# Optimization experiments

Hardware: AMD Instinct MI355X
Metric: run time of the kernel (lower is better)

The kernel has to match this reference:

```python
import jax, jax.numpy as jnp
import numpy as np

N_PROP = 1000
N_CLS = 81  # includes background class 0
IMG_H, IMG_W = 800, 1333
WX, WY, WW, WH = 10.0, 10.0, 5.0, 5.0
BBOX_XFORM_CLIP = float(np.log(1000.0 / 16.0))
SCORE_THRESH = 0.05
NMS_THRESH = 0.5
DET_PER_IMG = 100


def _decode(box_regression, proposals):
    widths = proposals[:, 2] - proposals[:, 0] + 1.0
    heights = proposals[:, 3] - proposals[:, 1] + 1.0
    ctr_x = proposals[:, 0] + 0.5 * widths
    ctr_y = proposals[:, 1] + 0.5 * heights
    rel = box_regression.reshape(box_regression.shape[0], -1, 4)  # [N, C, 4]
    dx = rel[..., 0] / WX
    dy = rel[..., 1] / WY
    dw = jnp.minimum(rel[..., 2] / WW, BBOX_XFORM_CLIP)
    dh = jnp.minimum(rel[..., 3] / WH, BBOX_XFORM_CLIP)
    pcx = dx * widths[:, None] + ctr_x[:, None]
    pcy = dy * heights[:, None] + ctr_y[:, None]
    pw = jnp.exp(dw) * widths[:, None]
    ph = jnp.exp(dh) * heights[:, None]
    return jnp.stack([pcx - 0.5 * pw, pcy - 0.5 * ph,
                      pcx + 0.5 * pw - 1.0, pcy + 0.5 * ph - 1.0], axis=-1)  # [N, C, 4]


def _clip_boxes(b, h, w):
    x1 = jnp.clip(b[..., 0], 0.0, w - 1.0)
    y1 = jnp.clip(b[..., 1], 0.0, h - 1.0)
    x2 = jnp.clip(b[..., 2], 0.0, w - 1.0)
    y2 = jnp.clip(b[..., 3], 0.0, h - 1.0)
    return jnp.stack([x1, y1, x2, y2], axis=-1)


def _nms_keep(boxes, scores, valid):
    # Greedy NMS for one class. boxes [N,4], scores [N], valid [N].
    # Returns keep mask in the ORIGINAL proposal order.
    n = scores.shape[0]
    order = jnp.argsort(-jnp.where(valid, scores, -jnp.inf))
    b = boxes[order]
    v = valid[order]
    x1, y1, x2, y2 = b[:, 0], b[:, 1], b[:, 2], b[:, 3]
    area = (x2 - x1 + 1.0) * (y2 - y1 + 1.0)
    iw = jnp.clip(jnp.minimum(x2[:, None], x2[None, :]) - jnp.maximum(x1[:, None], x1[None, :]) + 1.0, 0.0)
    ih = jnp.clip(jnp.minimum(y2[:, None], y2[None, :]) - jnp.maximum(y1[:, None], y1[None, :]) + 1.0, 0.0)
    inter = iw * ih
    iou = inter / (area[:, None] + area[None, :] - inter)
    idx = jnp.arange(n)

    def body(i, keep):
        sup = (iou[i] > NMS_THRESH) & (idx > i) & keep[i]
        return keep & ~sup

    keep = jax.lax.fori_loop(0, n, body, v)
    return jnp.zeros(n, dtype=bool).at[order].set(keep)


def _postprocess(class_logits, box_regression, proposal_boxes, image_h, image_w):
    prob = jax.nn.softmax(class_logits, axis=-1)             # [N, C]
    boxes = _decode(box_regression, proposal_boxes)           # [N, C, 4]
    boxes = _clip_boxes(boxes, float(image_h), float(image_w))
    scores_c = prob[:, 1:].T                                  # [C-1, N] skip background
    boxes_c = jnp.transpose(boxes[:, 1:, :], (1, 0, 2))       # [C-1, N, 4]
    valid = scores_c > SCORE_THRESH
    keep = jax.vmap(_nms_keep)(boxes_c, scores_c, valid)      # [C-1, N]
    masked = jnp.where(keep, scores_c, -jnp.inf)
    count = jnp.sum(keep)
    # torch.kthvalue(n - 100) == 101st largest kept score; keep scores >= it
    topv = jax.lax.top_k(masked.reshape(-1), DET_PER_IMG + 1)[0]
    image_thresh = jnp.where(count > DET_PER_IMG, topv[DET_PER_IMG], -jnp.inf)
    final = keep & (masked >= image_thresh)
    c1, n = scores_c.shape
    labels = jnp.broadcast_to(jnp.arange(1, c1 + 1, dtype=jnp.int32)[:, None], (c1, n))
    out_scores = jnp.where(final, scores_c, 0.0).reshape(-1)
    out_boxes = jnp.where(final[..., None], boxes_c, 0.0).reshape(-1, 4)
    out5 = jnp.concatenate([out_boxes, out_scores[:, None]], axis=1)  # [(C-1)*N, 5]
    return out5, jnp.where(final, labels, 0).reshape(-1), final.reshape(-1)


def setup_inputs() -> dict:
    key = jax.random.key(0)
    k1, k2, k3, k4 = jax.random.split(key, 4)
    # scale logits so a realistic fraction of softmax scores clears the 0.05 threshold
    class_logits = 3.0 * jax.random.normal(k1, (N_PROP, N_CLS), dtype=jnp.float32)
    box_regression = jax.random.normal(k2, (N_PROP, N_CLS * 4), dtype=jnp.float32)
    cxy = jax.random.uniform(k3, (N_PROP, 2), dtype=jnp.float32) * jnp.array([IMG_W, IMG_H], jnp.float32)
    wh = 16.0 + 284.0 * jax.random.uniform(k4, (N_PROP, 2), dtype=jnp.float32)
    x1y1 = jnp.clip(cxy - 0.5 * wh, 0.0)
    x2y2 = jnp.minimum(cxy + 0.5 * wh, jnp.array([IMG_W - 1.0, IMG_H - 1.0], jnp.float32))
    proposal_boxes = jnp.concatenate([x1y1, x2y2], axis=1)  # [N, 4] xyxy
    return {"class_logits": class_logits, "box_regression": box_regression,
            "proposal_boxes": proposal_boxes, "image_h": IMG_H, "image_w": IMG_W}


def reference(class_logits, box_regression, proposal_boxes, image_h, image_w):
    return _postprocess(class_logits, box_regression, proposal_boxes, image_h, image_w)
```

## Files before the change

kernel.cpp:

```cpp
#include <hip/hip_runtime.h>
#include <math.h>

#define N_PROP 1000
#define N_CLS  81
#define N_FG   80
#define SCORE_THRESH 0.05f
#define NMS_THRESH   0.5f
#define DET_PER_IMG  100
#define BBOX_CLIP    4.135166556742356f

#define LBL_OFF    400000
#define FIN_OFF    480000


__global__ __launch_bounds__(256)
void softmax_zero_kernel(const float* __restrict__ logits,
                         float* __restrict__ out,
                         int* __restrict__ count,
                         float* __restrict__ probT) {
    const int b = blockIdx.x;
    const int t = threadIdx.x;
    const int lane = t & 63;
    const int wave = t >> 6;
    if (b == 0 && t == 0) *count = 0;

    float4 z = make_float4(0.f, 0.f, 0.f, 0.f);
    float4* o4 = (float4*)out;
    for (int i = b * 256 + t; i < 140000; i += 250 * 256) o4[i] = z;

    const int n = b * 4 + wave;
    if (n < N_PROP) {
        const float* lrow = logits + (size_t)n * N_CLS;
        float v0 = lrow[lane];
        float v1 = (lane + 64 < N_CLS) ? lrow[lane + 64] : -INFINITY;
        float m = fmaxf(v0, v1);
        for (int off = 32; off; off >>= 1) m = fmaxf(m, __shfl_down(m, off));
        m = __shfl(m, 0);
        float e0 = expf(v0 - m);
        float e1 = (lane + 64 < N_CLS) ? expf(v1 - m) : 0.0f;
        float s = e0 + e1;
        for (int off = 32; off; off >>= 1) s += __shfl_down(s, off);
        s = __shfl(s, 0);
        if (lane >= 1)          probT[(size_t)(lane - 1) * N_PROP + n] = e0 / s;
        if (lane + 64 < N_CLS)  probT[(size_t)(lane + 63) * N_PROP + n] = e1 / s;
    }
}

__global__ __launch_bounds__(256)
void nms_kernel(const float* __restrict__ probT,
                const float* __restrict__ props,
                const float* __restrict__ reg,
                const int* __restrict__ ihp,
                const int* __restrict__ iwp,
                float* __restrict__ out,
                int* __restrict__ count,
                float* __restrict__ compact,
                int* __restrict__ svRow) {
    const int c = blockIdx.x;
    const int t = threadIdx.x;
    const int lane = t & 63;
    const int cls = c + 1;
    const unsigned long long lm = (1ull << lane) - 1ull;

    __shared__ float sSc[N_PROP];
    __shared__ int   sIdx[N_PROP];
    __shared__ int   sPos[N_PROP];
    __shared__ float sx1[N_PROP], sy1[N_PROP], sx2[N_PROP], sy2[N_PROP];
    __shared__ float sar[N_PROP], sSc2[N_PROP];
    __shared__ int   sJdx[N_PROP];
    __shared__ unsigned char sKeep[N_PROP];
    __shared__ unsigned long long sColMask[128][2];
    __shared__ int   shV;

    for (int j = t; j < N_PROP; j += 256) sSc[j] = probT[(size_t)c * N_PROP + j];
    __syncthreads();

    if (t < 64) {
        int V = 0;
        #pragma unroll
        for (int it = 0; it < 16; ++it) {
            int j = it * 64 + lane;
            float sc = (j < N_PROP) ? sSc[j] : -1.0f;
            bool val = (j < N_PROP) && (sc > SCORE_THRESH);
            unsigned long long mask = __ballot(val);
            if (val) { int p = V + __popcll(mask & lm); sSc[p] = sc; sIdx[p] = j; }
            V += __popcll(mask);
        }
        if (lane == 0) shV = V;
    }
    __syncthreads();
    const int V = shV;

    const float W1 = (float)iwp[0] - 1.0f;
    const float H1 = (float)ihp[0] - 1.0f;

    if (V <= 128) {
        if (t < V) {
            float s = sSc[t];
            int id = sIdx[t];
            int r = 0;
            for (int u = 0; u < V; ++u) {
                float su = sSc[u];
                r += (su > s) || (su == s && sIdx[u] < id);
            }
            float4 pr = *(const float4*)(props + (size_t)id * 4);
            float w  = pr.z - pr.x + 1.0f;
            float h  = pr.w - pr.y + 1.0f;
            float cx = pr.x + 0.5f * w;
            float cy = pr.y + 0.5f * h;
            float4 rr = *(const float4*)(reg + ((size_t)id * N_CLS + cls) * 4);
            float dx = rr.x / 10.0f;
            float dy = rr.y / 10.0f;
            float dw = fminf(rr.z / 5.0f, BBOX_CLIP);
            float dh = fminf(rr.w / 5.0f, BBOX_CLIP);
            float pcx = dx * w + cx;
            float pcy = dy * h + cy;
            float pw = expf(dw) * w;
            float ph = expf(dh) * h;
            float bx1 = fminf(fmaxf(pcx - 0.5f * pw, 0.0f), W1);
            float by1 = fminf(fmaxf(pcy - 0.5f * ph, 0.0f), H1);
            float bx2 = fminf(fmaxf(pcx + 0.5f * pw - 1.0f, 0.0f), W1);
            float by2 = fminf(fmaxf(pcy + 0.5f * ph - 1.0f, 0.0f), H1);
            sx1[r] = bx1; sy1[r] = by1; sx2[r] = bx2; sy2[r] = by2;
            sar[r] = (bx2 - bx1 + 1.0f) * (by2 - by1 + 1.0f);
            sSc2[r] = s;
            sJdx[r] = id;
        }
        __syncthreads();

        if (t < V) {
            const float X1 = sx1[t], Y1 = sy1[t], X2 = sx2[t], Y2 = sy2[t], A = sar[t];
            unsigned long long m0 = 0ull, m1 = 0ull;
            for (int r = 0; r < t; ++r) {
                float iw = fmaxf(fminf(sx2[r], X2) - fmaxf(sx1[r], X1) + 1.0f, 0.0f);
                float ih = fmaxf(fminf(sy2[r], Y2) - fmaxf(sy1[r], Y1) + 1.0f, 0.0f);
                float inter = iw * ih;
                float iou = inter / (sar[r] + A - inter);
                if (iou > NMS_THRESH) {
                    if (r < 64) m0 |= 1ull << r; else m1 |= 1ull << (r - 64);
                }
            }
            sColMask[t][0] = m0;
            sColMask[t][1] = m1;
        }
        __syncthreads();

        if (t < 64) {
            const bool hasA = (lane < V), hasB = (64 + lane < V);
            unsigned long long Mlo = 0ull, M2lo = 0ull, M2hi = 0ull;
            if (hasA) Mlo  = sColMask[lane][0];
            if (hasB) { M2lo = sColMask[64 + lane][0]; M2hi = sColMask[64 + lane][1]; }

            unsigned long long keep = 0ull, keep2 = 0ull;
            bool a = hasA, a2 = hasB;
            while (true) {
                unsigned long long b1 = __ballot(a);
                unsigned long long b2 = __ballot(a2);
                if (!(b1 | b2)) break;
                int r = b1 ? (__ffsll((long long)b1) - 1) : (64 + __ffsll((long long)b2) - 1);
                if (r < 64) {
                    keep |= 1ull << r;
                    if (a  && ((Mlo  >> r) & 1ull)) a  = false;
                    if (a2 && ((M2lo >> r) & 1ull)) a2 = false;
                    if (lane == r) a = false;
                } else {
                    int rr = r - 64;
                    keep2 |= 1ull << rr;
                    if (a2 && ((M2hi >> rr) & 1ull)) a2 = false;
                    if (lane == rr) a2 = false;
                }
            }

            int total = __popcll(keep) + __popcll(keep2);
            int base = 0;
            if (lane == 0 && total > 0) base = atomicAdd(count, total);
            base = __shfl(base, 0);
            if ((keep >> lane) & 1ull) {
                float sc = sSc2[lane];
                int row = c * N_PROP + sJdx[lane];
                size_t o = (size_t)row * 5;
                out[o + 0] = sx1[lane]; out[o + 1] = sy1[lane];
                out[o + 2] = sx2[lane]; out[o + 3] = sy2[lane];
                out[o + 4] = sc;
                out[LBL_OFF + row] = (float)cls;
                out[FIN_OFF + row] = 1.0f;
                int pos = base + __popcll(keep & lm);
                compact[pos] = sc; svRow[pos] = row;
            }
            if ((keep2 >> lane) & 1ull) {
                float sc = sSc2[64 + lane];
                int row = c * N_PROP + sJdx[64 + lane];
                size_t o = (size_t)row * 5;
                out[o + 0] = sx1[64 + lane]; out[o + 1] = sy1[64 + lane];
                out[o + 2] = sx2[64 + lane]; out[o + 3] = sy2[64 + lane];
                out[o + 4] = sc;
                out[LBL_OFF + row] = (float)cls;
                out[FIN_OFF + row] = 1.0f;
                int pos = base + __popcll(keep) + __popcll(keep2 & lm);
                compact[pos] = sc; svRow[pos] = row;
            }
        }
    } else {
        for (int v = t; v < V; v += 256) {
            float s = sSc[v];
            int id = sIdx[v];
            int r = 0;
            for (int u = 0; u < V; ++u) {
                float su = sSc[u];
                r += (su > s) || (su == s && sIdx[u] < id);
            }
            sPos[v] = r;
        }
        __syncthreads();
        for (int v = t; v < V; v += 256) {
            int r = sPos[v];
            int j = sIdx[v];
            float4 pr = *(const float4*)(props + (size_t)j * 4);
            float w  = pr.z - pr.x + 1.0f;
            float h  = pr.w - pr.y + 1.0f;
            float cx = pr.x + 0.5f * w;
            float cy = pr.y + 0.5f * h;
            float4 rr = *(const float4*)(reg + ((size_t)j * N_CLS + cls) * 4);
            float dx = rr.x / 10.0f;
            float dy = rr.y / 10.0f;
            float dw = fminf(rr.z / 5.0f, BBOX_CLIP);
            float dh = fminf(rr.w / 5.0f, BBOX_CLIP);
            float pcx = dx * w + cx;
            float pcy = dy * h + cy;
            float pw = expf(dw) * w;
            float ph = expf(dh) * h;
            float bx1 = fminf(fmaxf(pcx - 0.5f * pw, 0.0f), W1);
            float by1 = fminf(fmaxf(pcy - 0.5f * ph, 0.0f), H1);
            float bx2 = fminf(fmaxf(pcx + 0.5f * pw - 1.0f, 0.0f), W1);
            float by2 = fminf(fmaxf(pcy + 0.5f * ph - 1.0f, 0.0f), H1);
            sx1[r] = bx1; sy1[r] = by1; sx2[r] = bx2; sy2[r] = by2;
            sar[r] = (bx2 - bx1 + 1.0f) * (by2 - by1 + 1.0f);
            sSc2[r] = sSc[v];
            sJdx[r] = j;
            sKeep[r] = 1;
        }
        __syncthreads();
        for (int r = 0; r < V; ++r) {
            if (sKeep[r]) {
                const float X1 = sx1[r], Y1 = sy1[r], X2 = sx2[r], Y2 = sy2[r], A = sar[r];
                for (int v = r + 1 + t; v < V; v += 256) {
                    if (sKeep[v]) {
                        float iw = fmaxf(fminf(X2, sx2[v]) - fmaxf(X1, sx1[v]) + 1.0f, 0.0f);
                        float ih = fmaxf(fminf(Y2, sy2[v]) - fmaxf(Y1, sy1[v]) + 1.0f, 0.0f);
                        float inter = iw * ih;
                        float iou = inter / (A + sar[v] - inter);
                        if (iou > NMS_THRESH) sKeep[v] = 0;
                    }
                }
            }
            __syncthreads();
        }
        for (int vb = 0; vb < V; vb += 256) {
            int v = vb + t;
            bool k = (v < V) && sKeep[v];
            unsigned long long mask = __ballot(k);
            int cntw = __popcll(mask);
            int base = 0;
            if (lane == 0 && cntw > 0) base = atomicAdd(count, cntw);
            base = __shfl(base, 0);
            if (k) {
                int row = c * N_PROP + sJdx[v];
                size_t o = (size_t)row * 5;
                out[o + 0] = sx1[v]; out[o + 1] = sy1[v];
                out[o + 2] = sx2[v]; out[o + 3] = sy2[v];
                out[o + 4] = sSc2[v];
                out[LBL_OFF + row] = (float)cls;
                out[FIN_OFF + row] = 1.0f;
                int pos = base + __popcll(mask & lm);
                compact[pos] = sSc2[v];
                svRow[pos] = row;
            }
        }
    }
}

__global__ __launch_bounds__(256)
void finalize_kernel(float* __restrict__ out,
                     const float* __restrict__ compact,
                     const int* __restrict__ svRow,
                     const int* __restrict__ count) {
    __shared__ float lsc[8192];
    __shared__ float sTh;
    const int n = *count;
    const int t = threadIdx.x;
    const int lane = t & 63;

    if (n <= DET_PER_IMG) return;

    const bool useL = (n <= 8192);
    if (useL) {
        for (int i = t; i < n; i += 256) lsc[i] = compact[i];
    }
    __syncthreads();

    if (t < 64) {
        unsigned lo = 0x3D4CCCCCu, hi = 0x40000000u;
        while (hi - lo > 1u) {
            unsigned mid = lo + ((hi - lo) >> 1);
            float mv = __uint_as_float(mid);
            int cnt = 0;
            if (useL) {
                for (int i = lane; i < n; i += 64) cnt += (lsc[i] >= mv) ? 1 : 0;
            } else {
                for (int i = lane; i < n; i += 64) cnt += (compact[i] >= mv) ? 1 : 0;
            }
            for (int off = 32; off; off >>= 1) cnt += __shfl_xor(cnt, off);
            if (cnt >= DET_PER_IMG + 1) lo = mid; else hi = mid;
        }
        if (lane == 0) sTh = __uint_as_float(lo);
    }
    __syncthreads();
    const float th = sTh;

    for (int i = blockIdx.x * 256 + t; i < n; i += gridDim.x * 256) {
        float sc = compact[i];
        if (sc < th) {
            int row = svRow[i];
            size_t o = (size_t)row * 5;
            out[o + 0] = 0.0f;
            out[o + 1] = 0.0f;
            out[o + 2] = 0.0f;
            out[o + 3] = 0.0f;
            out[o + 4] = 0.0f;
            out[LBL_OFF + row] = 0.0f;
            out[FIN_OFF + row] = 0.0f;
        }
    }
}

extern "C" void kernel_launch(void* const* d_in, const int* in_sizes, int n_in,
                              void* d_out, int out_size, void* d_ws, size_t ws_size,
                              hipStream_t stream) {
    const float* logits = (const float*)d_in[0];
    const float* reg    = (const float*)d_in[1];
    const float* props  = (const float*)d_in[2];
    const int*   ihp    = (const int*)d_in[3];
    const int*   iwp    = (const int*)d_in[4];
    float* out = (float*)d_out;

    char* ws = (char*)d_ws;
    int*   count   = (int*)(ws + 0);
    float* probT   = (float*)(ws + 64);
    float* compact = (float*)(ws + 320064);
    int*   svRow   = (int*)(ws + 640064);

    softmax_zero_kernel<<<250, 256, 0, stream>>>(logits, out, count, probT);
    nms_kernel<<<N_FG, 256, 0, stream>>>(probT, props, reg, ihp, iwp,
                                         out, count, compact, svRow);
    finalize_kernel<<<16, 256, 0, stream>>>(out, compact, svRow, count);
}
```

Measured before the change: 66.96 us.

## Shrink NMS block to 128 threads, pool shared memory, fuse rank and decode loops

The per-class NMS kernel now runs with 128 threads instead of 256. Its separate shared arrays are merged into one aliased pool so the fast path and the fallback path reuse the same storage, and the rank computation is fused with box decoding, which drops the sPos array and one barrier. The aim is to cut shared-memory footprint and barrier cost, since most per-class work is small. The trade-off is less parallelism in the rank, suppression and output loops when a class has many valid candidates, and the fast path is still assumed to use at most 128 candidates.

Result: no change. 67.93 us (+1.5%).

```diff
diff --git a/kernel.cpp b/kernel.cpp
--- a/kernel.cpp
+++ b/kernel.cpp
@@ -46,7 +46,7 @@
     }
 }
 
-__global__ __launch_bounds__(256)
+__global__ __launch_bounds__(128)
 void nms_kernel(const float* __restrict__ probT,
                 const float* __restrict__ props,
                 const float* __restrict__ reg,
@@ -64,15 +64,16 @@
 
     __shared__ float sSc[N_PROP];
     __shared__ int   sIdx[N_PROP];
-    __shared__ int   sPos[N_PROP];
-    __shared__ float sx1[N_PROP], sy1[N_PROP], sx2[N_PROP], sy2[N_PROP];
-    __shared__ float sar[N_PROP], sSc2[N_PROP];
-    __shared__ int   sJdx[N_PROP];
-    __shared__ unsigned char sKeep[N_PROP];
+    __shared__ float sPool[8000];
     __shared__ unsigned long long sColMask[128][2];
     __shared__ int   shV;
 
-    for (int j = t; j < N_PROP; j += 256) sSc[j] = probT[(size_t)c * N_PROP + j];
+    float* sx1 = sPool;        float* sy1 = sPool + 128;
+    float* sx2 = sPool + 256;  float* sy2 = sPool + 384;
+    float* sar = sPool + 512;  float* sSc2 = sPool + 640;
+    int*   sJdx = (int*)(sPool + 768);
+
+    for (int j = t; j < N_PROP; j += 128) sSc[j] = probT[(size_t)c * N_PROP + j];
     __syncthreads();
 
     if (t < 64) {
@@ -201,7 +202,12 @@
             }
         }
     } else {
-        for (int v = t; v < V; v += 256) {
+        float* fx1 = sPool;          float* fy1 = sPool + 1000;
+        float* fx2 = sPool + 2000;   float* fy2 = sPool + 3000;
+        float* fa  = sPool + 4000;   float* fs  = sPool + 5000;
+        int*   fj  = (int*)(sPool + 6000);
+        int*   fk  = (int*)(sPool + 7000);
+        for (int v = t; v < V; v += 128) {
             float s = sSc[v];
             int id = sIdx[v];
             int r = 0;
@@ -209,18 +215,12 @@
                 float su = sSc[u];
                 r += (su > s) || (su == s && sIdx[u] < id);
             }
-            sPos[v] = r;
-        }
-        __syncthreads();
-        for (int v = t; v < V; v += 256) {
-            int r = sPos[v];
-            int j = sIdx[v];
-            float4 pr = *(const float4*)(props + (size_t)j * 4);
+            float4 pr = *(const float4*)(props + (size_t)id * 4);
             float w  = pr.z - pr.x + 1.0f;
             float h  = pr.w - pr.y + 1.0f;
             float cx = pr.x + 0.5f * w;
             float cy = pr.y + 0.5f * h;
-            float4 rr = *(const float4*)(reg + ((size_t)j * N_CLS + cls) * 4);
+            float4 rr = *(const float4*)(reg + ((size_t)id * N_CLS + cls) * 4);
             float dx = rr.x / 10.0f;
             float dy = rr.y / 10.0f;
             float dw = fminf(rr.z / 5.0f, BBOX_CLIP);
@@ -233,47 +233,67 @@
             float by1 = fminf(fmaxf(pcy - 0.5f * ph, 0.0f), H1);
             float bx2 = fminf(fmaxf(pcx + 0.5f * pw - 1.0f, 0.0f), W1);
             float by2 = fminf(fmaxf(pcy + 0.5f * ph - 1.0f, 0.0f), H1);
-            sx1[r] = bx1; sy1[r] = by1; sx2[r] = bx2; sy2[r] = by2;
-            sar[r] = (bx2 - bx1 + 1.0f) * (by2 - by1 + 1.0f);
-            sSc2[r] = sSc[v];
-            sJdx[r] = j;
-            sKeep[r] = 1;
+            fx1[r] = bx1; fy1[r] = by1; fx2[r] = bx2; fy2[r] = by2;
+            fa[r] = (bx2 - bx1 + 1.0f) * (by2 - by1 + 1.0f);
+            fs[r] = s; fj[r] = id; fk[r] = 1;
         }
         __syncthreads();
         for (int r = 0; r < V; ++r) {
-            if (sKeep[r]) {
-                const float X1 = sx1[r], Y1 = sy1[r], X2 = sx2[r], Y2 = sy2[r], A = sar[r];
-                for (int v = r + 1 + t; v < V; v += 256) {
-                    if (sKeep[v]) {
-                        float iw = fmaxf(fminf(X2, sx2[v]) - fmaxf(X1, sx1[v]) + 1.0f, 0.0f);
-                        float ih = fmaxf(fminf(Y2, sy2[v]) - fmaxf(Y1, sy1[v]) + 1.0f, 0.0f);
+            if (fk[r]) {
+                const float X1 = fx1[r], Y1 = fy1[r], X2 = fx2[r], Y2 = fy2[r], A = fa[r];
+                for (int v = r + 1 + t; v < V; v += 128) {
+                    if (fk[v]) {
+                        float iw = fmaxf(fminf(X2, fx2[v]) - fmaxf(X1, fx1[v]) + 1.0f, 0.0f);
+                        float ih = fmaxf(fminf(Y2, fy2[v]) - fmaxf(Y1, fy1[v]) + 1.0f, 0.0f);
                         float inter = iw * ih;
-                        float iou = inter / (A + sar[v] - inter);
-                        if (iou > NMS_THRESH) sKeep[v] = 0;
+                        float iou = inter / (A + fa[v] - inter);
+                        if (iou > NMS_THRESH) fk[v] = 0;
                     }
                 }
             }
             __syncthreads();
         }
-        for (int vb = 0; vb < V; vb += 256) {
+        for (int vb = 0; vb < V; vb += 128) {
             int v = vb + t;
-            bool k = (v < V) && sKeep[v];
+            bool k = (v < V) && fk[v];
             unsigned long long mask = __ballot(k);
-            int cntw = __popcll(mask);
-            int base = 0;
-            if (lane == 0 && cntw > 0) base = atomicAdd(count, cntw);
-            base = __shfl(base, 0);
-            if (k) {
-                int row = c * N_PROP + sJdx[v];
-                size_t o = (size_t)row * 5;
-                out[o + 0] = sx1[v]; out[o + 1] = sy1[v];
-                out[o + 2] = sx2[v]; out[o + 3] = sy2[v];
-                out[o + 4] = sSc2[v];
-                out[LBL_OFF + row] = (float)cls;
-                out[FIN_OFF + row] = 1.0f;
-                int pos = base + __popcll(mask & lm);
-                compact[pos] = sSc2[v];
-                svRow[pos] = row;
+            int half0 = 0;
+            if (t < 64) {
+                int cntw = __popcll(mask);
+                int base = 0;
+                if (lane == 0 && cntw > 0) base = atomicAdd(count, cntw);
+                base = __shfl(base, 0);
+                half0 = base;
+                if (k) {
+                    int row = c * N_PROP + fj[v];
+                    size_t o = (size_t)row * 5;
+                    out[o + 0] = fx1[v]; out[o + 1] = fy1[v];
+                    out[o + 2] = fx2[v]; out[o + 3] = fy2[v];
+                    out[o + 4] = fs[v];
+                    out[LBL_OFF + row] = (float)cls;
+                    out[FIN_OFF + row] = 1.0f;
+                    int pos = base + __popcll(mask & lm);
+                    compact[pos] = fs[v];
+                    svRow[pos] = row;
+                }
+            } else {
+                int cntw = __popcll(mask);
+                int base = 0;
+                if (lane == 0 && cntw > 0) base = atomicAdd(count, cntw);
+                base = __shfl(base, 0);
+                (void)half0;
+                if (k) {
+                    int row = c * N_PROP + fj[v];
+                    size_t o = (size_t)row * 5;
+                    out[o + 0] = fx1[v]; out[o + 1] = fy1[v];
+                    out[o + 2] = fx2[v]; out[o + 3] = fy2[v];
+                    out[o + 4] = fs[v];
+                    out[LBL_OFF + row] = (float)cls;
+                    out[FIN_OFF + row] = 1.0f;
+                    int pos = base + __popcll(mask & lm);
+                    compact[pos] = fs[v];
+                    svRow[pos] = row;
+                }
             }
         }
     }
@@ -350,7 +370,7 @@
     int*   svRow   = (int*)(ws + 640064);
 
     softmax_zero_kernel<<<250, 256, 0, stream>>>(logits, out, count, probT);
-    nms_kernel<<<N_FG, 256, 0, stream>>>(probT, props, reg, ihp, iwp,
+    nms_kernel<<<N_FG, 128, 0, stream>>>(probT, props, reg, ihp, iwp,
                                          out, count, compact, svRow);
     finalize_kernel<<<16, 256, 0, stream>>>(out, compact, svRow, count);
 }
```
